# Kernel optimization log

Measured on AMD Instinct MI355X. Metric: run time of the kernel, lower is better.

The kernel has to match this reference:

```python
import jax, jax.numpy as jnp
import numpy as np

WS = 8  # window size (module uses window_sizes as a scalar)


def setup_inputs() -> dict:
    key = jax.random.key(0)
    ks = jax.random.split(key, 4)
    b, c, h, w = 4, 128, 256, 256
    x = jax.random.normal(ks[0], (b, c, h, w), jnp.float32)
    w_qkv = jax.random.normal(ks[1], (3 * c, c), jnp.float32) * (1.0 / np.sqrt(c))
    w_dw = jax.random.normal(ks[2], (3 * c, 1, 3, 3), jnp.float32) * (1.0 / 3.0)
    w_proj = jax.random.normal(ks[3], (c, c), jnp.float32) * (1.0 / np.sqrt(c))
    temperature = jnp.ones((1, 1, 1), jnp.float32)
    return {"x": x, "w_qkv": w_qkv, "w_dw": w_dw, "w_proj": w_proj,
            "temperature": temperature}


def _window(t, ws):
    # b c (h dh) (w dw) -> b (h w) (dh dw) c
    b, c, H, W = t.shape
    t = t.reshape(b, c, H // ws, ws, W // ws, ws)
    return t.transpose(0, 2, 4, 3, 5, 1).reshape(b, (H // ws) * (W // ws), ws * ws, c)


def _unwindow(t, ws, H, W):
    # b (h w) (dh dw) c -> b c (h dh) (w dw)
    b = t.shape[0]
    c = t.shape[-1]
    t = t.reshape(b, H // ws, W // ws, ws, ws, c)
    return t.transpose(0, 5, 1, 3, 2, 4).reshape(b, c, H, W)


def reference(x, w_qkv, w_dw, w_proj, temperature):
    b, c, H, W = x.shape
    ws = WS
    sh = -ws // 2  # = -(ws//2) for even ws, matching torch.roll shifts
    x_ = jnp.roll(x, (sh, sh), axis=(2, 3))
    # 1x1 conv c -> 3c
    qkv = jnp.einsum('oc,bchw->bohw', w_qkv, x_)
    # depthwise 3x3, padding 1
    qkv = jax.lax.conv_general_dilated(
        qkv, w_dw, window_strides=(1, 1), padding=[(1, 1), (1, 1)],
        dimension_numbers=('NCHW', 'OIHW', 'NCHW'), feature_group_count=3 * c)
    q, k, v = jnp.split(qkv, 3, axis=1)
    q = _window(q, ws)  # [b, nW, ws*ws, c]
    k = _window(k, ws)
    v = _window(v, ws)
    # L2-normalize along channel dim (torch F.normalize, eps=1e-12)
    q = q / jnp.maximum(jnp.linalg.norm(q, axis=-1, keepdims=True), 1e-12)
    k = k / jnp.maximum(jnp.linalg.norm(k, axis=-1, keepdims=True), 1e-12)
    # channel-wise attention: [b, nW, c, c]
    attn = jnp.einsum('bnpc,bnpd->bncd', q, k) * temperature.reshape(())
    attn = jax.nn.relu(attn)
    out = jnp.einsum('bnpc,bncd->bnpd', v, attn)  # [b, nW, ws*ws, c]
    out = _unwindow(out, ws, H, W)
    out = jnp.roll(out, (ws // 2, ws // 2), axis=(2, 3))
    y = jnp.einsum('oc,bchw->bohw', w_proj, out)
    return (y, attn)
```

## Files before the change

kernel.cpp:

```cpp
#include <hip/hip_runtime.h>
#include <hip/hip_bf16.h>

constexpr int NB = 4;
constexpr int CC = 128;
constexpr int HW = 65536;

using bf16x8 = __attribute__((ext_vector_type(8))) short;
using f32x4  = __attribute__((ext_vector_type(4))) float;

__device__ __forceinline__ unsigned short f2bf(float f) {
  unsigned u = __builtin_bit_cast(unsigned, f);
  u += 0x7FFFu + ((u >> 16) & 1u);
  return (unsigned short)(u >> 16);
}
__device__ __forceinline__ float bf2f(unsigned short s) {
  return __builtin_bit_cast(float, (unsigned)s << 16);
}

__device__ __forceinline__ int swz128(int row, int b) { return row * 128 + (b ^ ((row & 7) << 4)); }
__device__ __forceinline__ int swz256(int row, int b) { return row * 256 + (b ^ ((row & 15) << 4)); }

__device__ __forceinline__ uint4 hload(const __hip_bfloat16* __restrict__ base,
                                       int ih0, int iw0, int idx) {
  int ch = idx / 30;
  int rem = idx - ch * 30;
  int r = rem / 3, c = rem - r * 3;
  int ii = ih0 - 1 + r, j0 = iw0 - 8 + c * 8;
  uint4 v = {0u, 0u, 0u, 0u};
  if (idx < 1920 && (unsigned)ii < 256u && (unsigned)j0 <= 248u)
    v = *(const uint4*)(base + (((size_t)ch) << 16) + (ii << 8) + j0);
  return v;
}
__device__ __forceinline__ void hstore(unsigned short* __restrict__ halo, int idx, uint4 v) {
  if (idx >= 1920) return;
  int ch = idx / 30;
  int rem = idx - ch * 30;
  int r = rem / 3, c = rem - r * 3;
  unsigned short* hrow = halo + ch * 168 + r * 16;
  if (c == 1) *(uint4*)hrow = v;
  else if (c == 0) hrow[9] = (unsigned short)(v.w >> 16);
  else hrow[8] = (unsigned short)(v.x & 0xFFFFu);
}

__device__ __forceinline__ void dw_row(const unsigned short* __restrict__ halo,
                                       const float* __restrict__ wd,
                                       int chl, int pr, float* __restrict__ outv) {
#pragma unroll
  for (int pc = 0; pc < 8; ++pc) outv[pc] = 0.f;
#pragma unroll
  for (int kr = 0; kr < 3; ++kr) {
    const unsigned short* hrow = halo + chl * 168 + (pr + kr) * 16;
    uint4 rw = *(const uint4*)hrow;
    float rv[10];
    rv[0] = bf2f((unsigned short)(rw.x & 0xFFFFu));
    rv[1] = bf2f((unsigned short)(rw.x >> 16));
    rv[2] = bf2f((unsigned short)(rw.y & 0xFFFFu));
    rv[3] = bf2f((unsigned short)(rw.y >> 16));
    rv[4] = bf2f((unsigned short)(rw.z & 0xFFFFu));
    rv[5] = bf2f((unsigned short)(rw.z >> 16));
    rv[6] = bf2f((unsigned short)(rw.w & 0xFFFFu));
    rv[7] = bf2f((unsigned short)(rw.w >> 16));
    rv[8] = bf2f(hrow[8]);
    rv[9] = bf2f(hrow[9]);
#pragma unroll
    for (int s = 0; s < 3; ++s) {
      float wv = wd[kr * 3 + s];
#pragma unroll
      for (int pc = 0; pc < 8; ++pc) {
        int m = pc + s - 1;
        float xv = (m < 0) ? rv[9] : rv[m];
        outv[pc] = fmaf(wv, xv, outv[pc]);
      }
    }
  }
}

template <bool SQ>
__device__ __forceinline__ void dw_half(const unsigned short* __restrict__ halo,
                                        const float* __restrict__ wdw_g,
                                        int g0, int ch_l, int pr, int half,
                                        float (*outv)[8], float* __restrict__ ssq) {
#pragma unroll
  for (int it = 0; it < 2; ++it) {
    int chl = (g0 + 2 * it) * 16 + ch_l;
    int chf = half * 64 + chl;
    float wd[9];
#pragma unroll
    for (int kk = 0; kk < 9; ++kk) wd[kk] = wdw_g[chf * 9 + kk];
    dw_row(halo, wd, chl, pr, outv[it]);
    if (SQ) {
#pragma unroll
      for (int pc = 0; pc < 8; ++pc)
        ssq[pc] = fmaf(outv[it][pc], outv[it][pc], ssq[pc]);
    }
  }
}

__global__ __launch_bounds__(256) void k_qkv_mfma(const float* __restrict__ x,
                                                  const float* __restrict__ wq,
                                                  __hip_bfloat16* __restrict__ qkv) {
  __shared__ unsigned short x_s[128 * 136];

  int blk = blockIdx.x;
  int b = blk >> 9, i = (blk >> 1) & 255, jh = blk & 1;
  int j0 = jh << 7;
  int si = (i + 4) & 255;
  int t = threadIdx.x;

  {
    int c0 = (t & 63) << 1;
    int jb = (t >> 6) << 5;
    const float* xr0 = x + (((size_t)(b * CC + c0)) << 16) + (si << 8);
    const float* xr1 = xr0 + HW;
#pragma unroll
    for (int u = 0; u < 8; ++u) {
      int jj = jb + (u << 2);
      int sj = j0 + jj + 4;
      float v0[4], v1[4];
      if (sj + 3 <= 255) {
        *(float4*)v0 = *(const float4*)(xr0 + sj);
        *(float4*)v1 = *(const float4*)(xr1 + sj);
      } else {
#pragma unroll
        for (int e = 0; e < 4; ++e) {
          int s = (sj + e) & 255;
          v0[e] = xr0[s];
          v1[e] = xr1[s];
        }
      }
#pragma unroll
      for (int e = 0; e < 4; ++e) {
        unsigned pk = (unsigned)f2bf(v0[e]) | ((unsigned)f2bf(v1[e]) << 16);
        *(unsigned*)&x_s[(jj + e) * 136 + c0] = pk;
      }
    }
  }
  __syncthreads();

  int w = t >> 6;
  int lane = t & 63;
  int col = lane & 15;
  int kg = lane >> 4;

#pragma unroll 1
  for (int oi = 0; oi < 3; ++oi) {
    int m0 = oi * 128 + w * 32;
    bf16x8 afr[2][4];
#pragma unroll
    for (int mt = 0; mt < 2; ++mt) {
      const float* wr = wq + (m0 + mt * 16 + col) * CC + kg * 8;
#pragma unroll
      for (int ks = 0; ks < 4; ++ks) {
        float wa[4], wb[4];
        *(float4*)wa = *(const float4*)(wr + ks * 32);
        *(float4*)wb = *(const float4*)(wr + ks * 32 + 4);
        bf16x8 f;
#pragma unroll
        for (int e = 0; e < 4; ++e) {
          f[e] = (short)f2bf(wa[e]);
          f[e + 4] = (short)f2bf(wb[e]);
        }
        afr[mt][ks] = f;
      }
    }
#pragma unroll 1
    for (int n = 0; n < 8; ++n) {
      int px = n * 16 + col;
      f32x4 acc0 = {0.f, 0.f, 0.f, 0.f};
      f32x4 acc1 = {0.f, 0.f, 0.f, 0.f};
#pragma unroll
      for (int ks = 0; ks < 4; ++ks) {
        bf16x8 bfr = *(const bf16x8*)&x_s[px * 136 + ks * 32 + kg * 8];
        acc0 = __builtin_amdgcn_mfma_f32_16x16x32_bf16(afr[0][ks], bfr, acc0, 0, 0, 0);
        acc1 = __builtin_amdgcn_mfma_f32_16x16x32_bf16(afr[1][ks], bfr, acc1, 0, 0, 0);
      }
      int j = j0 + n * 16 + col;
#pragma unroll
      for (int r = 0; r < 4; ++r) {
        int och0 = m0 + kg * 4 + r;
        int och1 = m0 + 16 + kg * 4 + r;
        int g0 = och0 >> 7, c0 = och0 & 127;
        int g1 = och1 >> 7, c1 = och1 & 127;
        qkv[(((size_t)((g0 * NB + b) * CC + c0)) << 16) + (i << 8) + j] =
            __float2bfloat16(acc0[r]);
        qkv[(((size_t)((g1 * NB + b) * CC + c1)) << 16) + (i << 8) + j] =
            __float2bfloat16(acc1[r]);
      }
    }
  }
}

__global__ __launch_bounds__(256) void k_fused(const __hip_bfloat16* __restrict__ qkv,
                                               const float* __restrict__ wdw,
                                               const float* __restrict__ temp_p,
                                               const float* __restrict__ wp,
                                               float* __restrict__ attn_out,
                                               float* __restrict__ y) {
  __shared__ __align__(16) char smem[54272];
  unsigned short* halo = (unsigned short*)smem;
  char* RB = smem + 21504;
  char* RC = smem + 21504 + 16384;

  int bid = blockIdx.x;
  int blk = ((bid & 7) << 9) + (bid >> 3);
  int b = blk >> 10, n = blk & 1023;
  int ih0 = (n >> 5) << 3, iw0 = (n & 31) << 3;
  int t = threadIdx.x;
  int ch_l = t & 15;
  int wv = t >> 6, lane = t & 63;
  int col = lane & 15, kg = lane >> 4;
  int giw = (t >> 4) & 3;
  int pr = 2 * wv + (giw & 1);
  int g0 = giw >> 1;
  float tau = temp_p[0];
  const __hip_bfloat16* qb = qkv + (((size_t)(b * CC)) << 16);
  const __hip_bfloat16* kb = qb + (((size_t)(NB * CC)) << 16);
  const __hip_bfloat16* vb = qb + (((size_t)(2 * NB * CC)) << 16);
  const size_t HALF = ((size_t)64) << 16;

  uint4 pre[8];
  float outv[4][8];
  float ssq[8];

#pragma unroll
  for (int it = 0; it < 8; ++it) {
    int idx = it * 256 + t;
    hstore(halo, idx, hload(qb, ih0, iw0, idx));
  }
  __syncthreads();
#pragma unroll
  for (int it = 0; it < 8; ++it) pre[it] = hload(qb + HALF, ih0, iw0, it * 256 + t);
#pragma unroll
  for (int pc = 0; pc < 8; ++pc) ssq[pc] = 0.f;
  dw_half<true>(halo, wdw, g0, ch_l, pr, 0, &outv[0], ssq);
  __syncthreads();
#pragma unroll
  for (int it = 0; it < 8; ++it) hstore(halo, it * 256 + t, pre[it]);
  __syncthreads();
#pragma unroll
  for (int it = 0; it < 8; ++it) pre[it] = hload(kb, ih0, iw0, it * 256 + t);
  dw_half<true>(halo, wdw, g0, ch_l, pr, 1, &outv[2], ssq);
  {
    float psv[8];
#pragma unroll
    for (int pc = 0; pc < 8; ++pc) {
      float s = ssq[pc];
      s += __shfl_xor(s, 1); s += __shfl_xor(s, 2);
      s += __shfl_xor(s, 4); s += __shfl_xor(s, 8);
      s += __shfl_xor(s, 32);
      psv[pc] = 1.f / fmaxf(sqrtf(s), 1e-12f);
    }
#pragma unroll
    for (int tk = 0; tk < 4; ++tk) {
      int chf = (tk >> 1) * 64 + (g0 + 2 * (tk & 1)) * 16 + ch_l;
      unsigned short o8[8];
#pragma unroll
      for (int pc = 0; pc < 8; ++pc) o8[pc] = f2bf(outv[tk][pc] * psv[pc]);
      *(uint4*)(RB + swz128(chf, pr * 16)) = *(const uint4*)o8;
    }
  }
  __syncthreads();
#pragma unroll
  for (int it = 0; it < 8; ++it) hstore(halo, it * 256 + t, pre[it]);
  __syncthreads();
#pragma unroll
  for (int it = 0; it < 8; ++it) pre[it] = hload(kb + HALF, ih0, iw0, it * 256 + t);
#pragma unroll
  for (int pc = 0; pc < 8; ++pc) ssq[pc] = 0.f;
  dw_half<true>(halo, wdw + CC * 9, g0, ch_l, pr, 0, &outv[0], ssq);
  __syncthreads();
#pragma unroll
  for (int it = 0; it < 8; ++it) hstore(halo, it * 256 + t, pre[it]);
  __syncthreads();
#pragma unroll
  for (int it = 0; it < 8; ++it) pre[it] = hload(vb, ih0, iw0, it * 256 + t);
  dw_half<true>(halo, wdw + CC * 9, g0, ch_l, pr, 1, &outv[2], ssq);
  {
    float psv[8];
#pragma unroll
    for (int pc = 0; pc < 8; ++pc) {
      float s = ssq[pc];
      s += __shfl_xor(s, 1); s += __shfl_xor(s, 2);
      s += __shfl_xor(s, 4); s += __shfl_xor(s, 8);
      s += __shfl_xor(s, 32);
      psv[pc] = tau / fmaxf(sqrtf(s), 1e-12f);
    }
#pragma unroll
    for (int tk = 0; tk < 4; ++tk) {
      int chf = (tk >> 1) * 64 + (g0 + 2 * (tk & 1)) * 16 + ch_l;
      unsigned short o8[8];
#pragma unroll
      for (int pc = 0; pc < 8; ++pc) o8[pc] = f2bf(outv[tk][pc] * psv[pc]);
      *(uint4*)(RC + swz128(chf, pr * 16)) = *(const uint4*)o8;
    }
  }
  __syncthreads();
#pragma unroll
  for (int it = 0; it < 8; ++it) hstore(halo, it * 256 + t, pre[it]);
  __syncthreads();
#pragma unroll
  for (int it = 0; it < 8; ++it) pre[it] = hload(vb + HALF, ih0, iw0, it * 256 + t);
  int c0 = wv * 32;
  f32x4 pa0[8], pa1[8];
  {
    bf16x8 afr[2][2];
#pragma unroll
    for (int mt = 0; mt < 2; ++mt)
#pragma unroll
      for (int ks = 0; ks < 2; ++ks)
        afr[mt][ks] = *(const bf16x8*)(RB + swz128(c0 + mt * 16 + col, ks * 64 + kg * 16));
    float* ao = attn_out + ((size_t)blk << 14);
#pragma unroll
    for (int dt = 0; dt < 8; ++dt) {
      bf16x8 b0 = *(const bf16x8*)(RC + swz128(dt * 16 + col, kg * 16));
      bf16x8 b1 = *(const bf16x8*)(RC + swz128(dt * 16 + col, 64 + kg * 16));
      f32x4 a0 = {0.f, 0.f, 0.f, 0.f};
      f32x4 a1 = {0.f, 0.f, 0.f, 0.f};
      a0 = __builtin_amdgcn_mfma_f32_16x16x32_bf16(afr[0][0], b0, a0, 0, 0, 0);
      a0 = __builtin_amdgcn_mfma_f32_16x16x32_bf16(afr[0][1], b1, a0, 0, 0, 0);
      a1 = __builtin_amdgcn_mfma_f32_16x16x32_bf16(afr[1][0], b0, a1, 0, 0, 0);
      a1 = __builtin_amdgcn_mfma_f32_16x16x32_bf16(afr[1][1], b1, a1, 0, 0, 0);
#pragma unroll
      for (int r = 0; r < 4; ++r) {
        a0[r] = fmaxf(a0[r], 0.f);
        a1[r] = fmaxf(a1[r], 0.f);
        ao[((c0 + kg * 4 + r) << 7) + dt * 16 + col] = a0[r];
        ao[((c0 + 16 + kg * 4 + r) << 7) + dt * 16 + col] = a1[r];
      }
      pa0[dt] = a0;
      pa1[dt] = a1;
    }
  }
  __syncthreads();
  {
    float vo[2][8];
    dw_half<false>(halo, wdw + 2 * CC * 9, g0, ch_l, pr, 0, vo, nullptr);
#pragma unroll
    for (int it = 0; it < 2; ++it) {
      int chf = (g0 + 2 * it) * 16 + ch_l;
#pragma unroll
      for (int pc = 0; pc < 8; ++pc)
        *(unsigned short*)(RB + swz256(pr * 8 + pc, chf * 2)) = f2bf(vo[it][pc]);
    }
  }
  if (wv < 2) {
#pragma unroll
    for (int dt = 0; dt < 8; ++dt)
#pragma unroll
      for (int r = 0; r < 4; ++r) {
        int d = dt * 16 + col;
        *(unsigned short*)(RC + swz128(d, (c0 + kg * 4 + r) * 2)) = f2bf(pa0[dt][r]);
        *(unsigned short*)(RC + swz128(d, (c0 + 16 + kg * 4 + r) * 2)) = f2bf(pa1[dt][r]);
      }
  }
  __syncthreads();
#pragma unroll
  for (int it = 0; it < 8; ++it) hstore(halo, it * 256 + t, pre[it]);
  f32x4 pacc[8];
#pragma unroll
  for (int dt = 0; dt < 8; ++dt) pacc[dt] = {0.f, 0.f, 0.f, 0.f};
#pragma unroll
  for (int ks = 0; ks < 2; ++ks) {
    bf16x8 va = *(const bf16x8*)(RB + swz256(wv * 16 + col, ks * 64 + kg * 16));
#pragma unroll
    for (int dt = 0; dt < 8; ++dt) {
      bf16x8 bf = *(const bf16x8*)(RC + swz128(dt * 16 + col, (ks & 1) * 64 + kg * 16));
      pacc[dt] = __builtin_amdgcn_mfma_f32_16x16x32_bf16(va, bf, pacc[dt], 0, 0, 0);
    }
  }
  __syncthreads();
  {
    float vo[2][8];
    dw_half<false>(halo, wdw + 2 * CC * 9, g0, ch_l, pr, 1, vo, nullptr);
#pragma unroll
    for (int it = 0; it < 2; ++it) {
      int chf = 64 + (g0 + 2 * it) * 16 + ch_l;
#pragma unroll
      for (int pc = 0; pc < 8; ++pc)
        *(unsigned short*)(RB + swz256(pr * 8 + pc, chf * 2)) = f2bf(vo[it][pc]);
    }
  }
  if (wv >= 2) {
    int cl0 = c0 - 64;
#pragma unroll
    for (int dt = 0; dt < 8; ++dt)
#pragma unroll
      for (int r = 0; r < 4; ++r) {
        int d = dt * 16 + col;
        *(unsigned short*)(RC + swz128(d, (cl0 + kg * 4 + r) * 2)) = f2bf(pa0[dt][r]);
        *(unsigned short*)(RC + swz128(d, (cl0 + 16 + kg * 4 + r) * 2)) = f2bf(pa1[dt][r]);
      }
  }
  __syncthreads();
#pragma unroll
  for (int ks = 2; ks < 4; ++ks) {
    bf16x8 va = *(const bf16x8*)(RB + swz256(wv * 16 + col, ks * 64 + kg * 16));
#pragma unroll
    for (int dt = 0; dt < 8; ++dt) {
      bf16x8 bf = *(const bf16x8*)(RC + swz128(dt * 16 + col, (ks & 1) * 64 + kg * 16));
      pacc[dt] = __builtin_amdgcn_mfma_f32_16x16x32_bf16(va, bf, pacc[dt], 0, 0, 0);
    }
  }
  __syncthreads();
#pragma unroll
  for (int dt = 0; dt < 8; ++dt)
#pragma unroll
    for (int r = 0; r < 4; ++r)
      *(unsigned short*)(RB + swz256(wv * 16 + kg * 4 + r, (dt * 16 + col) * 2)) =
          f2bf(pacc[dt][r]);
  __syncthreads();
  {
    int p = wv * 16 + col;
    bf16x8 bfr[4];
#pragma unroll
    for (int ks = 0; ks < 4; ++ks)
      bfr[ks] = *(const bf16x8*)(RB + swz256(p, ks * 64 + kg * 16));
    int i_f = (((n >> 5) << 3) + (p >> 3) + 4) & 255;
    int j_f = (((n & 31) << 3) + (p & 7) + 4) & 255;
    float* yp = y + (((size_t)b * CC) << 16) + (i_f << 8) + j_f;
#pragma unroll
    for (int mt = 0; mt < 8; ++mt) {
      bf16x8 afr[4];
      const float* wr = wp + (mt * 16 + col) * CC + kg * 8;
#pragma unroll
      for (int ks = 0; ks < 4; ++ks) {
        float wa[4], wb[4];
        *(float4*)wa = *(const float4*)(wr + ks * 32);
        *(float4*)wb = *(const float4*)(wr + ks * 32 + 4);
        bf16x8 f;
#pragma unroll
        for (int e = 0; e < 4; ++e) {
          f[e] = (short)f2bf(wa[e]);
          f[e + 4] = (short)f2bf(wb[e]);
        }
        afr[ks] = f;
      }
      f32x4 acc = {0.f, 0.f, 0.f, 0.f};
#pragma unroll
      for (int ks = 0; ks < 4; ++ks)
        acc = __builtin_amdgcn_mfma_f32_16x16x32_bf16(afr[ks], bfr[ks], acc, 0, 0, 0);
#pragma unroll
      for (int r = 0; r < 4; ++r) {
        int och = mt * 16 + kg * 4 + r;
        yp[(size_t)och << 16] = acc[r];
      }
    }
  }
}

extern "C" void kernel_launch(void* const* d_in, const int* in_sizes, int n_in,
                              void* d_out, int out_size, void* d_ws, size_t ws_size,
                              hipStream_t stream) {
  const float* x = (const float*)d_in[0];
  const float* w_qkv = (const float*)d_in[1];
  const float* w_dw = (const float*)d_in[2];
  const float* w_proj = (const float*)d_in[3];
  const float* temp = (const float*)d_in[4];
  float* y = (float*)d_out;
  float* attn = (float*)d_out + (size_t)NB * CC * HW;

  __hip_bfloat16* qkv = (__hip_bfloat16*)d_ws;

  k_qkv_mfma<<<2048, 256, 0, stream>>>(x, w_qkv, qkv);
  k_fused<<<4096, 256, 0, stream>>>(qkv, w_dw, temp, w_proj, attn, y);
}
```

Measured before the change: 795.9 us.

## Load depthwise-conv halos directly into registers instead of staging through LDS

The fused attention kernel no longer stages each 64-channel q/k/v halo tile in shared memory. Each thread now loads its three input rows plus left and right edge pixels straight from global memory into registers, computes all four of its channels at once, and combines the per-pixel norm partial sums through a small shared buffer. This removes the halo shared-memory buffer and many barriers and shrinks LDS use, which should help occupancy. In exchange it raises register pressure and issues more overlapping, partly redundant global loads that rely on cache.

```diff
diff --git a/kernel.cpp b/kernel.cpp
--- a/kernel.cpp
+++ b/kernel.cpp
@@ -20,37 +20,35 @@
 __device__ __forceinline__ int swz128(int row, int b) { return row * 128 + (b ^ ((row & 7) << 4)); }
 __device__ __forceinline__ int swz256(int row, int b) { return row * 256 + (b ^ ((row & 15) << 4)); }
 
-__device__ __forceinline__ uint4 hload(const __hip_bfloat16* __restrict__ base,
-                                       int ih0, int iw0, int idx) {
-  int ch = idx / 30;
-  int rem = idx - ch * 30;
-  int r = rem / 3, c = rem - r * 3;
-  int ii = ih0 - 1 + r, j0 = iw0 - 8 + c * 8;
-  uint4 v = {0u, 0u, 0u, 0u};
-  if (idx < 1920 && (unsigned)ii < 256u && (unsigned)j0 <= 248u)
-    v = *(const uint4*)(base + (((size_t)ch) << 16) + (ii << 8) + j0);
-  return v;
-}
-__device__ __forceinline__ void hstore(unsigned short* __restrict__ halo, int idx, uint4 v) {
-  if (idx >= 1920) return;
-  int ch = idx / 30;
-  int rem = idx - ch * 30;
-  int r = rem / 3, c = rem - r * 3;
-  unsigned short* hrow = halo + ch * 168 + r * 16;
-  if (c == 1) *(uint4*)hrow = v;
-  else if (c == 0) hrow[9] = (unsigned short)(v.w >> 16);
-  else hrow[8] = (unsigned short)(v.x & 0xFFFFu);
-}
-
-__device__ __forceinline__ void dw_row(const unsigned short* __restrict__ halo,
-                                       const float* __restrict__ wd,
-                                       int chl, int pr, float* __restrict__ outv) {
+__device__ __forceinline__ void dw_load3(const __hip_bfloat16* __restrict__ base,
+                                         int ch, int ih0, int iw0, int pr,
+                                         uint4* __restrict__ m,
+                                         unsigned* __restrict__ lr) {
+#pragma unroll
+  for (int kr = 0; kr < 3; ++kr) {
+    int ii = ih0 + pr - 1 + kr;
+    uint4 mv = {0u, 0u, 0u, 0u};
+    unsigned lo = 0, hi = 0;
+    if ((unsigned)ii < 256u) {
+      const __hip_bfloat16* row = base + (((size_t)ch) << 16) + (ii << 8);
+      mv = *(const uint4*)(row + iw0);
+      if (iw0 > 0)   lo = (unsigned)__builtin_bit_cast(unsigned short, row[iw0 - 1]);
+      if (iw0 < 248) hi = (unsigned)__builtin_bit_cast(unsigned short, row[iw0 + 8]);
+    }
+    m[kr] = mv;
+    lr[kr] = lo | (hi << 16);
+  }
+}
+
+__device__ __forceinline__ void dw_regs(const uint4* __restrict__ m,
+                                        const unsigned* __restrict__ lr,
+                                        const float* __restrict__ wd,
+                                        float* __restrict__ outv) {
 #pragma unroll
   for (int pc = 0; pc < 8; ++pc) outv[pc] = 0.f;
 #pragma unroll
   for (int kr = 0; kr < 3; ++kr) {
-    const unsigned short* hrow = halo + chl * 168 + (pr + kr) * 16;
-    uint4 rw = *(const uint4*)hrow;
+    uint4 rw = m[kr];
     float rv[10];
     rv[0] = bf2f((unsigned short)(rw.x & 0xFFFFu));
     rv[1] = bf2f((unsigned short)(rw.x >> 16));
@@ -60,38 +58,17 @@
     rv[5] = bf2f((unsigned short)(rw.z >> 16));
     rv[6] = bf2f((unsigned short)(rw.w & 0xFFFFu));
     rv[7] = bf2f((unsigned short)(rw.w >> 16));
-    rv[8] = bf2f(hrow[8]);
-    rv[9] = bf2f(hrow[9]);
+    rv[8] = bf2f((unsigned short)(lr[kr] >> 16));
+    rv[9] = bf2f((unsigned short)(lr[kr] & 0xFFFFu));
 #pragma unroll
     for (int s = 0; s < 3; ++s) {
       float wv = wd[kr * 3 + s];
 #pragma unroll
       for (int pc = 0; pc < 8; ++pc) {
-        int m = pc + s - 1;
-        float xv = (m < 0) ? rv[9] : rv[m];
+        int mm = pc + s - 1;
+        float xv = (mm < 0) ? rv[9] : rv[mm];
         outv[pc] = fmaf(wv, xv, outv[pc]);
       }
-    }
-  }
-}
-
-template <bool SQ>
-__device__ __forceinline__ void dw_half(const unsigned short* __restrict__ halo,
-                                        const float* __restrict__ wdw_g,
-                                        int g0, int ch_l, int pr, int half,
-                                        float (*outv)[8], float* __restrict__ ssq) {
-#pragma unroll
-  for (int it = 0; it < 2; ++it) {
-    int chl = (g0 + 2 * it) * 16 + ch_l;
-    int chf = half * 64 + chl;
-    float wd[9];
-#pragma unroll
-    for (int kk = 0; kk < 9; ++kk) wd[kk] = wdw_g[chf * 9 + kk];
-    dw_row(halo, wd, chl, pr, outv[it]);
-    if (SQ) {
-#pragma unroll
-      for (int pc = 0; pc < 8; ++pc)
-        ssq[pc] = fmaf(outv[it][pc], outv[it][pc], ssq[pc]);
     }
   }
 }
@@ -196,110 +173,128 @@
                                                const float* __restrict__ wp,
                                                float* __restrict__ attn_out,
                                                float* __restrict__ y) {
-  __shared__ __align__(16) char smem[54272];
-  unsigned short* halo = (unsigned short*)smem;
-  char* RB = smem + 21504;
-  char* RC = smem + 21504 + 16384;
+  __shared__ __align__(16) char smem[33792];
+  char* RB = smem;
+  char* RC = smem + 16384;
+  float* sq = (float*)(smem + 32768);
 
   int bid = blockIdx.x;
   int blk = ((bid & 7) << 9) + (bid >> 3);
   int b = blk >> 10, n = blk & 1023;
   int ih0 = (n >> 5) << 3, iw0 = (n & 31) << 3;
   int t = threadIdx.x;
-  int ch_l = t & 15;
+  int ch_l = t & 15, grp = t >> 4;
+  int pr = grp & 7, contrib = grp >> 3;
   int wv = t >> 6, lane = t & 63;
   int col = lane & 15, kg = lane >> 4;
-  int giw = (t >> 4) & 3;
-  int pr = 2 * wv + (giw & 1);
-  int g0 = giw >> 1;
   float tau = temp_p[0];
   const __hip_bfloat16* qb = qkv + (((size_t)(b * CC)) << 16);
   const __hip_bfloat16* kb = qb + (((size_t)(NB * CC)) << 16);
   const __hip_bfloat16* vb = qb + (((size_t)(2 * NB * CC)) << 16);
-  const size_t HALF = ((size_t)64) << 16;
-
-  uint4 pre[8];
+
+  uint4 m[12];
+  unsigned lr[12];
   float outv[4][8];
   float ssq[8];
 
 #pragma unroll
-  for (int it = 0; it < 8; ++it) {
-    int idx = it * 256 + t;
-    hstore(halo, idx, hload(qb, ih0, iw0, idx));
-  }
-  __syncthreads();
-#pragma unroll
-  for (int it = 0; it < 8; ++it) pre[it] = hload(qb + HALF, ih0, iw0, it * 256 + t);
+  for (int itk = 0; itk < 4; ++itk) {
+    int ch = ((contrib + 2 * itk) << 4) + ch_l;
+    dw_load3(qb, ch, ih0, iw0, pr, &m[itk * 3], &lr[itk * 3]);
+  }
 #pragma unroll
   for (int pc = 0; pc < 8; ++pc) ssq[pc] = 0.f;
-  dw_half<true>(halo, wdw, g0, ch_l, pr, 0, &outv[0], ssq);
-  __syncthreads();
-#pragma unroll
-  for (int it = 0; it < 8; ++it) hstore(halo, it * 256 + t, pre[it]);
-  __syncthreads();
-#pragma unroll
-  for (int it = 0; it < 8; ++it) pre[it] = hload(kb, ih0, iw0, it * 256 + t);
-  dw_half<true>(halo, wdw, g0, ch_l, pr, 1, &outv[2], ssq);
+#pragma unroll
+  for (int itk = 0; itk < 4; ++itk) {
+    int ch = ((contrib + 2 * itk) << 4) + ch_l;
+    float wd[9];
+#pragma unroll
+    for (int kk = 0; kk < 9; ++kk) wd[kk] = wdw[ch * 9 + kk];
+    dw_regs(&m[itk * 3], &lr[itk * 3], wd, outv[itk]);
+#pragma unroll
+    for (int pc = 0; pc < 8; ++pc) ssq[pc] = fmaf(outv[itk][pc], outv[itk][pc], ssq[pc]);
+  }
+#pragma unroll
+  for (int pc = 0; pc < 8; ++pc) {
+    float s = ssq[pc];
+    s += __shfl_xor(s, 1); s += __shfl_xor(s, 2);
+    s += __shfl_xor(s, 4); s += __shfl_xor(s, 8);
+    ssq[pc] = s;
+  }
+  if (ch_l == 0) {
+#pragma unroll
+    for (int pc = 0; pc < 8; ++pc) sq[contrib * 64 + pr * 8 + pc] = ssq[pc];
+  }
+  __syncthreads();
+
+  {
+    uint4 m2[12];
+    unsigned lr2[12];
+#pragma unroll
+    for (int itk = 0; itk < 4; ++itk) {
+      int ch = ((contrib + 2 * itk) << 4) + ch_l;
+      dw_load3(kb, ch, ih0, iw0, pr, &m2[itk * 3], &lr2[itk * 3]);
+    }
+    {
+      float psv[8];
+#pragma unroll
+      for (int pc = 0; pc < 8; ++pc) {
+        float s = sq[pr * 8 + pc] + sq[64 + pr * 8 + pc];
+        psv[pc] = 1.f / fmaxf(sqrtf(s), 1e-12f);
+      }
+#pragma unroll
+      for (int itk = 0; itk < 4; ++itk) {
+        int ch = ((contrib + 2 * itk) << 4) + ch_l;
+        unsigned short o8[8];
+#pragma unroll
+        for (int pc = 0; pc < 8; ++pc) o8[pc] = f2bf(outv[itk][pc] * psv[pc]);
+        *(uint4*)(RB + swz128(ch, pr * 16)) = *(const uint4*)o8;
+      }
+    }
+#pragma unroll
+    for (int pc = 0; pc < 8; ++pc) ssq[pc] = 0.f;
+#pragma unroll
+    for (int itk = 0; itk < 4; ++itk) {
+      int ch = ((contrib + 2 * itk) << 4) + ch_l;
+      float wd[9];
+#pragma unroll
+      for (int kk = 0; kk < 9; ++kk) wd[kk] = wdw[(CC + ch) * 9 + kk];
+      dw_regs(&m2[itk * 3], &lr2[itk * 3], wd, outv[itk]);
+#pragma unroll
+      for (int pc = 0; pc < 8; ++pc) ssq[pc] = fmaf(outv[itk][pc], outv[itk][pc], ssq[pc]);
+    }
+  }
+#pragma unroll
+  for (int pc = 0; pc < 8; ++pc) {
+    float s = ssq[pc];
+    s += __shfl_xor(s, 1); s += __shfl_xor(s, 2);
+    s += __shfl_xor(s, 4); s += __shfl_xor(s, 8);
+    ssq[pc] = s;
+  }
+  if (ch_l == 0) {
+#pragma unroll
+    for (int pc = 0; pc < 8; ++pc) sq[128 + contrib * 64 + pr * 8 + pc] = ssq[pc];
+  }
+  __syncthreads();
+
   {
     float psv[8];
 #pragma unroll
     for (int pc = 0; pc < 8; ++pc) {
-      float s = ssq[pc];
-      s += __shfl_xor(s, 1); s += __shfl_xor(s, 2);
-      s += __shfl_xor(s, 4); s += __shfl_xor(s, 8);
-      s += __shfl_xor(s, 32);
-      psv[pc] = 1.f / fmaxf(sqrtf(s), 1e-12f);
-    }
-#pragma unroll
-    for (int tk = 0; tk < 4; ++tk) {
-      int chf = (tk >> 1) * 64 + (g0 + 2 * (tk & 1)) * 16 + ch_l;
+      float s = sq[128 + pr * 8 + pc] + sq[192 + pr * 8 + pc];
+      psv[pc] = tau / fmaxf(sqrtf(s), 1e-12f);
+    }
+#pragma unroll
+    for (int itk = 0; itk < 4; ++itk) {
+      int ch = ((contrib + 2 * itk) << 4) + ch_l;
       unsigned short o8[8];
 #pragma unroll
-      for (int pc = 0; pc < 8; ++pc) o8[pc] = f2bf(outv[tk][pc] * psv[pc]);
-      *(uint4*)(RB + swz128(chf, pr * 16)) = *(const uint4*)o8;
-    }
-  }
-  __syncthreads();
-#pragma unroll
-  for (int it = 0; it < 8; ++it) hstore(halo, it * 256 + t, pre[it]);
-  __syncthreads();
-#pragma unroll
-  for (int it = 0; it < 8; ++it) pre[it] = hload(kb + HALF, ih0, iw0, it * 256 + t);
-#pragma unroll
-  for (int pc = 0; pc < 8; ++pc) ssq[pc] = 0.f;
-  dw_half<true>(halo, wdw + CC * 9, g0, ch_l, pr, 0, &outv[0], ssq);
-  __syncthreads();
-#pragma unroll
-  for (int it = 0; it < 8; ++it) hstore(halo, it * 256 + t, pre[it]);
-  __syncthreads();
-#pragma unroll
-  for (int it = 0; it < 8; ++it) pre[it] = hload(vb, ih0, iw0, it * 256 + t);
-  dw_half<true>(halo, wdw + CC * 9, g0, ch_l, pr, 1, &outv[2], ssq);
-  {
-    float psv[8];
-#pragma unroll
-    for (int pc = 0; pc < 8; ++pc) {
-      float s = ssq[pc];
-      s += __shfl_xor(s, 1); s += __shfl_xor(s, 2);
-      s += __shfl_xor(s, 4); s += __shfl_xor(s, 8);
-      s += __shfl_xor(s, 32);
-      psv[pc] = tau / fmaxf(sqrtf(s), 1e-12f);
-    }
-#pragma unroll
-    for (int tk = 0; tk < 4; ++tk) {
-      int chf = (tk >> 1) * 64 + (g0 + 2 * (tk & 1)) * 16 + ch_l;
-      unsigned short o8[8];
-#pragma unroll
-      for (int pc = 0; pc < 8; ++pc) o8[pc] = f2bf(outv[tk][pc] * psv[pc]);
-      *(uint4*)(RC + swz128(chf, pr * 16)) = *(const uint4*)o8;
-    }
-  }
-  __syncthreads();
-#pragma unroll
-  for (int it = 0; it < 8; ++it) hstore(halo, it * 256 + t, pre[it]);
-  __syncthreads();
-#pragma unroll
-  for (int it = 0; it < 8; ++it) pre[it] = hload(vb + HALF, ih0, iw0, it * 256 + t);
+      for (int pc = 0; pc < 8; ++pc) o8[pc] = f2bf(outv[itk][pc] * psv[pc]);
+      *(uint4*)(RC + swz128(ch, pr * 16)) = *(const uint4*)o8;
+    }
+  }
+  __syncthreads();
+
   int c0 = wv * 32;
   f32x4 pa0[8], pa1[8];
   {
@@ -331,17 +326,24 @@
       pa1[dt] = a1;
     }
   }
-  __syncthreads();
-  {
-    float vo[2][8];
-    dw_half<false>(halo, wdw + 2 * CC * 9, g0, ch_l, pr, 0, vo, nullptr);
-#pragma unroll
-    for (int it = 0; it < 2; ++it) {
-      int chf = (g0 + 2 * it) * 16 + ch_l;
-#pragma unroll
-      for (int pc = 0; pc < 8; ++pc)
-        *(unsigned short*)(RB + swz256(pr * 8 + pc, chf * 2)) = f2bf(vo[it][pc]);
-    }
+#pragma unroll
+  for (int itk = 0; itk < 4; ++itk) {
+    int ch = ((contrib + 2 * itk) << 4) + ch_l;
+    dw_load3(vb, ch, ih0, iw0, pr, &m[itk * 3], &lr[itk * 3]);
+  }
+  __syncthreads();
+
+#pragma unroll
+  for (int itk = 0; itk < 4; ++itk) {
+    int ch = ((contrib + 2 * itk) << 4) + ch_l;
+    float wd[9];
+#pragma unroll
+    for (int kk = 0; kk < 9; ++kk) wd[kk] = wdw[(2 * CC + ch) * 9 + kk];
+    float vo[8];
+    dw_regs(&m[itk * 3], &lr[itk * 3], wd, vo);
+#pragma unroll
+    for (int pc = 0; pc < 8; ++pc)
+      *(unsigned short*)(RB + swz256(pr * 8 + pc, ch * 2)) = f2bf(vo[pc]);
   }
   if (wv < 2) {
 #pragma unroll
@@ -354,8 +356,7 @@
       }
   }
   __syncthreads();
-#pragma unroll
-  for (int it = 0; it < 8; ++it) hstore(halo, it * 256 + t, pre[it]);
+
   f32x4 pacc[8];
 #pragma unroll
   for (int dt = 0; dt < 8; ++dt) pacc[dt] = {0.f, 0.f, 0.f, 0.f};
@@ -369,17 +370,7 @@
     }
   }
   __syncthreads();
-  {
-    float vo[2][8];
-    dw_half<false>(halo, wdw + 2 * CC * 9, g0, ch_l, pr, 1, vo, nullptr);
-#pragma unroll
-    for (int it = 0; it < 2; ++it) {
-      int chf = 64 + (g0 + 2 * it) * 16 + ch_l;
-#pragma unroll
-      for (int pc = 0; pc < 8; ++pc)
-        *(unsigned short*)(RB + swz256(pr * 8 + pc, chf * 2)) = f2bf(vo[it][pc]);
-    }
-  }
+
   if (wv >= 2) {
     int cl0 = c0 - 64;
 #pragma unroll
@@ -392,6 +383,7 @@
       }
   }
   __syncthreads();
+
 #pragma unroll
   for (int ks = 2; ks < 4; ++ks) {
     bf16x8 va = *(const bf16x8*)(RB + swz256(wv * 16 + col, ks * 64 + kg * 16));
@@ -402,6 +394,7 @@
     }
   }
   __syncthreads();
+
 #pragma unroll
   for (int dt = 0; dt < 8; ++dt)
 #pragma unroll
@@ -409,6 +402,7 @@
       *(unsigned short*)(RB + swz256(wv * 16 + kg * 4 + r, (dt * 16 + col) * 2)) =
           f2bf(pacc[dt][r]);
   __syncthreads();
+
   {
     int p = wv * 16 + col;
     bf16x8 bfr[4];
```

After: 666.0 us. 1.2x faster.
